# Optimization experiments

Measured on AMD Instinct MI355X. Metric: run time of the kernel, lower is better.

The kernel has to match this reference:

```python
import jax, jax.numpy as jnp
import numpy as np
import math

B, S, D, H = 32, 512, 1024, 1024


def setup_inputs() -> dict:
    key = jax.random.key(0)
    k_feats, k_wih, k_whh, k_bih, k_bhh = jax.random.split(key, 5)
    stdv = 1.0 / math.sqrt(H)
    u = lambda k, shape: jax.random.uniform(k, shape, jnp.float32, -stdv, stdv)
    return {
        "feats": jax.random.normal(k_feats, (B, S, D), jnp.float32),
        "weight_ih": u(k_wih, (3 * H, D)),
        "weight_hh": u(k_whh, (3 * H, H)),
        "bias_ih": u(k_bih, (3 * H,)),
        "bias_hh": u(k_bhh, (3 * H,)),
    }


def reference(feats, weight_ih, weight_hh, bias_ih, bias_hh):
    b, s, d = feats.shape
    h_dim = weight_hh.shape[1]
    # Precompute input projections for all timesteps in one GEMM: [B,S,3H]
    gi_all = jnp.einsum('bsd,gd->bsg', feats, weight_ih) + bias_ih

    def step(h, gi_t):
        gh = h @ weight_hh.T + bias_hh  # [B,3H]
        i_r, i_i, i_n = jnp.split(gi_t, 3, axis=-1)
        h_r, h_i, h_n = jnp.split(gh, 3, axis=-1)
        resetgate = jax.nn.sigmoid(i_r + h_r)
        inputgate = jax.nn.sigmoid(i_i + h_i)
        newgate = jnp.tanh(i_n + resetgate * h_n)
        hy = newgate + inputgate * (h - newgate)
        return hy, hy

    h0 = jnp.zeros((b, h_dim), feats.dtype)
    h_last, outs = jax.lax.scan(step, h0, jnp.swapaxes(gi_all, 0, 1))  # outs: [S,B,H]
    output = jnp.swapaxes(outs, 0, 1)  # [B,S,H]
    return output, h_last
```

## Files before the change

### kernel.cpp

```cpp
#include <hip/hip_runtime.h>

#define B_  32
#define S_  512
#define D_  1024
#define H_  1024
#define G3  3072

typedef __attribute__((ext_vector_type(8))) short  short8;
typedef __attribute__((ext_vector_type(4))) float  floatx4;

__device__ __forceinline__ unsigned short f2bf(float f) {
    unsigned int u = __builtin_bit_cast(unsigned int, f);
    u = (u + 0x7FFFu + ((u >> 16) & 1u)) >> 16;
    return (unsigned short)u;
}
__device__ __forceinline__ float bf2f(unsigned short h) {
    unsigned int u = ((unsigned int)h) << 16;
    return __builtin_bit_cast(float, u);
}
__device__ __forceinline__ float fsigmoid(float x) {
    float e = __builtin_amdgcn_exp2f(-1.4426950408889634f * x);
    return __builtin_amdgcn_rcpf(1.f + e);
}
__device__ __forceinline__ float ftanh(float x) {
    float e = __builtin_amdgcn_exp2f(2.8853900817779268f * x);
    return 1.f - 2.f * __builtin_amdgcn_rcpf(e + 1.f);
}

__global__ __launch_bounds__(256) void convert_kernel(
    const float* __restrict__ wih, const float* __restrict__ whh,
    unsigned short* __restrict__ wih_h,
    unsigned short* __restrict__ whh_h, unsigned short* __restrict__ whh_l,
    unsigned int* __restrict__ hbuf ,
    int* __restrict__ cnt ) {
    int tid = blockIdx.x * 256 + threadIdx.x;
    int i4 = tid * 4;
    if (i4 < 3145728) {
        float4 w = *(const float4*)(wih + i4);
        ushort4 o;
        o.x = f2bf(w.x); o.y = f2bf(w.y); o.z = f2bf(w.z); o.w = f2bf(w.w);
        *(ushort4*)(wih_h + i4) = o;

        float4 v = *(const float4*)(whh + i4);
        ushort4 h;
        h.x = f2bf(v.x); h.y = f2bf(v.y); h.z = f2bf(v.z); h.w = f2bf(v.w);
        ushort4 l;
        l.x = f2bf(v.x - bf2f(h.x)); l.y = f2bf(v.y - bf2f(h.y));
        l.z = f2bf(v.z - bf2f(h.z)); l.w = f2bf(v.w - bf2f(h.w));
        *(ushort4*)(whh_h + i4) = h;
        *(ushort4*)(whh_l + i4) = l;
    }
    if (tid < 16384) {
        uint4 z; z.x = z.y = z.z = z.w = 0;
        *(uint4*)(hbuf + tid * 4) = z;
    }
    if (tid < 32) {
        int4 z4; z4.x = z4.y = z4.z = z4.w = 0;
        *(int4*)(cnt + tid * 4) = z4;
    }
}

#define BM 128
#define BN 128
#define BK 32
#define LDA 40

__global__ __launch_bounds__(256, 2) void gi_gemm(
    const float* __restrict__ feats,
    const unsigned short* __restrict__ wih_h,
    const float* __restrict__ bias_ih,
    unsigned short* __restrict__ gi) {
    __shared__ unsigned short As[BM * LDA];
    __shared__ unsigned short Bs[BN * LDA];

    int bx = blockIdx.x;
    int nb = bx % (G3 / BN);
    int mb = bx / (G3 / BN);
    int m0 = mb * BM, n0 = nb * BN;
    int tid = threadIdx.x;
    int lane = tid & 63, wave = tid >> 6;
    int quad = lane >> 4, l15 = lane & 15;
    int wm = (wave >> 1) * 64, wn = (wave & 1) * 64;

    floatx4 acc[4][4];
#pragma unroll
    for (int i = 0; i < 4; ++i)
#pragma unroll
        for (int j = 0; j < 4; ++j) acc[i][j] = (floatx4){0.f, 0.f, 0.f, 0.f};

    float bias[4];
#pragma unroll
    for (int j = 0; j < 4; ++j) bias[j] = bias_ih[n0 + wn + j * 16 + l15];

    int srow = tid >> 1, shalf = tid & 1;
    const float* aptr = feats + (size_t)(m0 + srow) * D_ + shalf * 16;
    const unsigned short* bptr = wih_h + (size_t)(n0 + srow) * D_ + shalf * 16;
    unsigned short* as = As + srow * LDA + shalf * 16;
    unsigned short* bs = Bs + srow * LDA + shalf * 16;

    for (int kt = 0; kt < D_ / BK; ++kt) {
        int k0 = kt * BK;
        float4 a0 = *(const float4*)(aptr + k0);
        float4 a1 = *(const float4*)(aptr + k0 + 4);
        float4 a2 = *(const float4*)(aptr + k0 + 8);
        float4 a3 = *(const float4*)(aptr + k0 + 12);
        uint4 bA = *(const uint4*)(bptr + k0);
        uint4 bB = *(const uint4*)(bptr + k0 + 8);

        union { unsigned short u16[16]; uint4 v[2]; } pk;
        pk.u16[0] = f2bf(a0.x);  pk.u16[1] = f2bf(a0.y);
        pk.u16[2] = f2bf(a0.z);  pk.u16[3] = f2bf(a0.w);
        pk.u16[4] = f2bf(a1.x);  pk.u16[5] = f2bf(a1.y);
        pk.u16[6] = f2bf(a1.z);  pk.u16[7] = f2bf(a1.w);
        pk.u16[8] = f2bf(a2.x);  pk.u16[9] = f2bf(a2.y);
        pk.u16[10] = f2bf(a2.z); pk.u16[11] = f2bf(a2.w);
        pk.u16[12] = f2bf(a3.x); pk.u16[13] = f2bf(a3.y);
        pk.u16[14] = f2bf(a3.z); pk.u16[15] = f2bf(a3.w);

        *(uint4*)as = pk.v[0];
        *(uint4*)(as + 8) = pk.v[1];
        *(uint4*)bs = bA;
        *(uint4*)(bs + 8) = bB;
        __syncthreads();

        short8 af[4], bf[4];
#pragma unroll
        for (int i = 0; i < 4; ++i)
            af[i] = *(const short8*)(As + (wm + i * 16 + l15) * LDA + quad * 8);
#pragma unroll
        for (int j = 0; j < 4; ++j)
            bf[j] = *(const short8*)(Bs + (wn + j * 16 + l15) * LDA + quad * 8);
#pragma unroll
        for (int i = 0; i < 4; ++i)
#pragma unroll
            for (int j = 0; j < 4; ++j)
                acc[i][j] = __builtin_amdgcn_mfma_f32_16x16x32_bf16(
                    af[i], bf[j], acc[i][j], 0, 0, 0);
        __syncthreads();
    }

#pragma unroll
    for (int i = 0; i < 4; ++i)
#pragma unroll
        for (int j = 0; j < 4; ++j)
#pragma unroll
            for (int r = 0; r < 4; ++r) {
                int m = m0 + wm + i * 16 + quad * 4 + r;
                int n = n0 + wn + j * 16 + l15;
                gi[(size_t)m * G3 + n] = f2bf(acc[i][j][r] + bias[j]);
            }
}

__global__ __launch_bounds__(512, 2) void gru_rec(
    const unsigned short* __restrict__ gi,
    const unsigned short* __restrict__ whh_h,
    const unsigned short* __restrict__ whh_l,
    const float* __restrict__ bias_hh,
    unsigned int* __restrict__ hbuf,
    int* __restrict__ cnt,
    float* __restrict__ out) {
    __shared__ floatx4 parts[8][3][64];

    int jg = blockIdx.x >> 1, mt = blockIdx.x & 1;
    int tid = threadIdx.x;
    int ks = tid >> 6, lane = tid & 63;
    int quad = lane >> 4, l15 = lane & 15;
    int j = jg * 16 + l15;

    short8 wfh[3][4], wfl[3][4];
#pragma unroll
    for (int g = 0; g < 3; ++g)
#pragma unroll
        for (int ki = 0; ki < 4; ++ki) {
            size_t off = (size_t)(g * H_ + j) * H_ + ks * 128 + ki * 32 + quad * 8;
            wfh[g][ki] = *(const short8*)(whh_h + off);
            wfl[g][ki] = *(const short8*)(whh_l + off);
        }

    float bhh[3] = {0.f, 0.f, 0.f};
    float hreg[4] = {0.f, 0.f, 0.f, 0.f};
    if (ks == 0) {
#pragma unroll
        for (int g = 0; g < 3; ++g) bhh[g] = bias_hh[g * H_ + j];
    }

    const int arow = mt * 16 + l15;
    const int kbase = ks * 128 + quad * 8;
    int* const cbase = cnt + mt * 64;

    for (int t = 0; t < S_; ++t) {
        unsigned short giu[3][4];
        if (ks == 0) {
#pragma unroll
            for (int g = 0; g < 3; ++g)
#pragma unroll
                for (int r = 0; r < 4; ++r) {
                    int b = mt * 16 + quad * 4 + r;
                    giu[g][r] = gi[((size_t)b * S_ + t) * G3 + g * H_ + j];
                }
        }

        if (t > 0) {
            if (ks == 0) {
                int v = __hip_atomic_load(cbase + lane, __ATOMIC_RELAXED,
                                          __HIP_MEMORY_SCOPE_AGENT);
                while (!__all(v >= t)) {
                    __builtin_amdgcn_s_sleep(1);
                    v = __hip_atomic_load(cbase + lane, __ATOMIC_RELAXED,
                                          __HIP_MEMORY_SCOPE_AGENT);
                }
            }
            __syncthreads();
        }

        const unsigned int* hc = hbuf + ((t & 1) << 15);
        unsigned int* hn = hbuf + (((t & 1) ^ 1) << 15);

        short8 ah[4], al[4];
#pragma unroll
        for (int ki = 0; ki < 4; ++ki) {
            const unsigned long long* p =
                (const unsigned long long*)(hc + arow * H_ + kbase + ki * 32);
            unsigned long long q[4];
#pragma unroll
            for (int c = 0; c < 4; ++c)
                q[c] = __hip_atomic_load(p + c, __ATOMIC_RELAXED,
                                         __HIP_MEMORY_SCOPE_AGENT);
            short8 av, lv;
#pragma unroll
            for (int c = 0; c < 4; ++c) {
                unsigned int u0 = (unsigned int)q[c];
                unsigned int u1 = (unsigned int)(q[c] >> 32);
                av[2 * c]     = (short)(u0 & 0xffffu);
                av[2 * c + 1] = (short)(u1 & 0xffffu);
                lv[2 * c]     = (short)(u0 >> 16);
                lv[2 * c + 1] = (short)(u1 >> 16);
            }
            ah[ki] = av;
            al[ki] = lv;
        }

        floatx4 acc[3];
#pragma unroll
        for (int g = 0; g < 3; ++g) acc[g] = (floatx4){0.f, 0.f, 0.f, 0.f};
#pragma unroll
        for (int ki = 0; ki < 4; ++ki)
#pragma unroll
            for (int g = 0; g < 3; ++g) {
                acc[g] = __builtin_amdgcn_mfma_f32_16x16x32_bf16(ah[ki], wfh[g][ki], acc[g], 0, 0, 0);
                acc[g] = __builtin_amdgcn_mfma_f32_16x16x32_bf16(ah[ki], wfl[g][ki], acc[g], 0, 0, 0);
                acc[g] = __builtin_amdgcn_mfma_f32_16x16x32_bf16(al[ki], wfh[g][ki], acc[g], 0, 0, 0);
            }
#pragma unroll
        for (int g = 0; g < 3; ++g) parts[ks][g][lane] = acc[g];
        __syncthreads();

        float hy[4];
        if (ks == 0) {
            floatx4 gh[3];
#pragma unroll
            for (int g = 0; g < 3; ++g) {
                floatx4 s = parts[0][g][lane];
#pragma unroll
                for (int w = 1; w < 8; ++w) s += parts[w][g][lane];
                gh[g] = s;
            }
#pragma unroll
            for (int r = 0; r < 4; ++r) {
                int b = mt * 16 + quad * 4 + r;
                float rg = fsigmoid(bf2f(giu[0][r]) + gh[0][r] + bhh[0]);
                float zg = fsigmoid(bf2f(giu[1][r]) + gh[1][r] + bhh[1]);
                float ng = ftanh(bf2f(giu[2][r]) + rg * (gh[2][r] + bhh[2]));
                float h = ng + zg * (hreg[r] - ng);
                hreg[r] = h;
                hy[r] = h;
                unsigned short hh = f2bf(h);
                unsigned int pk = (unsigned int)hh |
                                  ((unsigned int)f2bf(h - bf2f(hh)) << 16);
                __hip_atomic_store(hn + b * H_ + j, pk, __ATOMIC_RELAXED,
                                   __HIP_MEMORY_SCOPE_AGENT);
            }
            asm volatile("s_waitcnt vmcnt(0)" ::: "memory");
            if (tid == 0)
                __hip_atomic_store(cbase + jg, t + 1, __ATOMIC_RELAXED,
                                   __HIP_MEMORY_SCOPE_AGENT);
#pragma unroll
            for (int r = 0; r < 4; ++r) {
                int b = mt * 16 + quad * 4 + r;
                __builtin_nontemporal_store(hy[r], out + ((size_t)b * S_ + t) * H_ + j);
                if (t == S_ - 1)
                    __builtin_nontemporal_store(hy[r], out + (size_t)B_ * S_ * H_ + (size_t)b * H_ + j);
            }
        }
    }
}

extern "C" void kernel_launch(void* const* d_in, const int* in_sizes, int n_in,
                              void* d_out, int out_size, void* d_ws, size_t ws_size,
                              hipStream_t stream) {
    const float* feats = (const float*)d_in[0];
    const float* wih   = (const float*)d_in[1];
    const float* whh   = (const float*)d_in[2];
    const float* bih   = (const float*)d_in[3];
    const float* bhh   = (const float*)d_in[4];
    float* out = (float*)d_out;

    unsigned short* wih_h = (unsigned short*)d_ws;
    unsigned short* whh_h = wih_h + (size_t)3145728;
    unsigned short* whh_l = whh_h + (size_t)3145728;
    unsigned short* gi    = whh_l + (size_t)3145728;
    unsigned int*   hbuf  = (unsigned int*)(gi + (size_t)16384 * G3);
    int*            cnt   = (int*)(hbuf + 65536);

    hipLaunchKernelGGL(convert_kernel, dim3(3072), dim3(256), 0, stream,
                       wih, whh, wih_h, whh_h, whh_l, hbuf, cnt);
    hipLaunchKernelGGL(gi_gemm, dim3(3072), dim3(256), 0, stream,
                       feats, wih_h, bih, gi);

    void* args[] = {(void*)&gi, (void*)&whh_h, (void*)&whh_l,
                    (void*)&bhh, (void*)&hbuf, (void*)&cnt, (void*)&out};
    hipLaunchCooperativeKernel((const void*)gru_rec, dim3(128), dim3(512),
                               args, 0, stream);
}
```

Baseline: 3.457 ms.

## Distribute gate math across four waves and poll per-wave flags directly

The GRU gate epilogue, previously done by wave 0 alone for four batch rows, is now split across four waves that each handle one row. Each wave posts its own completion flag. Every wave spins on just the flags for its K-slice, which replaces the wave-0 poll plus __syncthreads barrier and removes the s_sleep. The partial-sum LDS buffer is double-buffered by timestep so the next step's writes cannot race the current reduction. The aim is a shorter serial critical path per timestep, at the cost of more polling traffic and a larger flag array.

```diff
diff --git a/kernel.cpp b/kernel.cpp
--- a/kernel.cpp
+++ b/kernel.cpp
@@ -54,7 +54,7 @@
         uint4 z; z.x = z.y = z.z = z.w = 0;
         *(uint4*)(hbuf + tid * 4) = z;
     }
-    if (tid < 32) {
+    if (tid < 128) {
         int4 z4; z4.x = z4.y = z4.z = z4.w = 0;
         *(int4*)(cnt + tid * 4) = z4;
     }
@@ -159,7 +159,7 @@
     unsigned int* __restrict__ hbuf,
     int* __restrict__ cnt,
     float* __restrict__ out) {
-    __shared__ floatx4 parts[8][3][64];
+    __shared__ floatx4 parts[2][8][3][64];
 
     int jg = blockIdx.x >> 1, mt = blockIdx.x & 1;
     int tid = threadIdx.x;
@@ -177,40 +177,41 @@
             wfl[g][ki] = *(const short8*)(whh_l + off);
         }
 
-    float bhh[3] = {0.f, 0.f, 0.f};
-    float hreg[4] = {0.f, 0.f, 0.f, 0.f};
-    if (ks == 0) {
-#pragma unroll
-        for (int g = 0; g < 3; ++g) bhh[g] = bias_hh[g * H_ + j];
-    }
-
     const int arow = mt * 16 + l15;
     const int kbase = ks * 128 + quad * 8;
-    int* const cbase = cnt + mt * 64;
+
+    const int q = ks;
+    const bool gater = (ks < 4);
+    const int grow = mt * 16 + quad * 4 + q;
+    float bhh0 = 0.f, bhh1 = 0.f, bhh2 = 0.f, hreg = 0.f;
+    if (gater) {
+        bhh0 = bias_hh[j];
+        bhh1 = bias_hh[H_ + j];
+        bhh2 = bias_hh[2 * H_ + j];
+    }
+
+    int* const pollbase = cnt + mt * 256 + ks * 32;
+    int* const myflag   = cnt + mt * 256 + (jg >> 3) * 32 + (jg & 7) * 4 + q;
 
     for (int t = 0; t < S_; ++t) {
-        unsigned short giu[3][4];
-        if (ks == 0) {
-#pragma unroll
-            for (int g = 0; g < 3; ++g)
-#pragma unroll
-                for (int r = 0; r < 4; ++r) {
-                    int b = mt * 16 + quad * 4 + r;
-                    giu[g][r] = gi[((size_t)b * S_ + t) * G3 + g * H_ + j];
-                }
+        unsigned short giu0 = 0, giu1 = 0, giu2 = 0;
+        if (gater) {
+            size_t gb = ((size_t)grow * S_ + t) * G3 + j;
+            giu0 = gi[gb];
+            giu1 = gi[gb + H_];
+            giu2 = gi[gb + 2 * H_];
         }
 
         if (t > 0) {
-            if (ks == 0) {
-                int v = __hip_atomic_load(cbase + lane, __ATOMIC_RELAXED,
-                                          __HIP_MEMORY_SCOPE_AGENT);
-                while (!__all(v >= t)) {
-                    __builtin_amdgcn_s_sleep(1);
-                    v = __hip_atomic_load(cbase + lane, __ATOMIC_RELAXED,
-                                          __HIP_MEMORY_SCOPE_AGENT);
-                }
-            }
-            __syncthreads();
+            int v = (lane < 32)
+                ? __hip_atomic_load(pollbase + lane, __ATOMIC_RELAXED,
+                                    __HIP_MEMORY_SCOPE_AGENT) : t;
+            while (!__all(v >= t)) {
+                v = (lane < 32)
+                    ? __hip_atomic_load(pollbase + lane, __ATOMIC_RELAXED,
+                                        __HIP_MEMORY_SCOPE_AGENT) : t;
+            }
+            asm volatile("" ::: "memory");
         }
 
         const unsigned int* hc = hbuf + ((t & 1) << 15);
@@ -221,16 +222,16 @@
         for (int ki = 0; ki < 4; ++ki) {
             const unsigned long long* p =
                 (const unsigned long long*)(hc + arow * H_ + kbase + ki * 32);
-            unsigned long long q[4];
+            unsigned long long qd[4];
 #pragma unroll
             for (int c = 0; c < 4; ++c)
-                q[c] = __hip_atomic_load(p + c, __ATOMIC_RELAXED,
-                                         __HIP_MEMORY_SCOPE_AGENT);
+                qd[c] = __hip_atomic_load(p + c, __ATOMIC_RELAXED,
+                                          __HIP_MEMORY_SCOPE_AGENT);
             short8 av, lv;
 #pragma unroll
             for (int c = 0; c < 4; ++c) {
-                unsigned int u0 = (unsigned int)q[c];
-                unsigned int u1 = (unsigned int)(q[c] >> 32);
+                unsigned int u0 = (unsigned int)qd[c];
+                unsigned int u1 = (unsigned int)(qd[c] >> 32);
                 av[2 * c]     = (short)(u0 & 0xffffu);
                 av[2 * c + 1] = (short)(u1 & 0xffffu);
                 lv[2 * c]     = (short)(u0 >> 16);
@@ -251,46 +252,41 @@
                 acc[g] = __builtin_amdgcn_mfma_f32_16x16x32_bf16(ah[ki], wfl[g][ki], acc[g], 0, 0, 0);
                 acc[g] = __builtin_amdgcn_mfma_f32_16x16x32_bf16(al[ki], wfh[g][ki], acc[g], 0, 0, 0);
             }
-#pragma unroll
-        for (int g = 0; g < 3; ++g) parts[ks][g][lane] = acc[g];
+        const int pb = t & 1;
+#pragma unroll
+        for (int g = 0; g < 3; ++g) parts[pb][ks][g][lane] = acc[g];
         __syncthreads();
 
-        float hy[4];
-        if (ks == 0) {
+        if (gater) {
             floatx4 gh[3];
 #pragma unroll
             for (int g = 0; g < 3; ++g) {
-                floatx4 s = parts[0][g][lane];
-#pragma unroll
-                for (int w = 1; w < 8; ++w) s += parts[w][g][lane];
+                floatx4 s = parts[pb][0][g][lane];
+#pragma unroll
+                for (int w = 1; w < 8; ++w) s += parts[pb][w][g][lane];
                 gh[g] = s;
             }
-#pragma unroll
-            for (int r = 0; r < 4; ++r) {
-                int b = mt * 16 + quad * 4 + r;
-                float rg = fsigmoid(bf2f(giu[0][r]) + gh[0][r] + bhh[0]);
-                float zg = fsigmoid(bf2f(giu[1][r]) + gh[1][r] + bhh[1]);
-                float ng = ftanh(bf2f(giu[2][r]) + rg * (gh[2][r] + bhh[2]));
-                float h = ng + zg * (hreg[r] - ng);
-                hreg[r] = h;
-                hy[r] = h;
-                unsigned short hh = f2bf(h);
-                unsigned int pk = (unsigned int)hh |
-                                  ((unsigned int)f2bf(h - bf2f(hh)) << 16);
-                __hip_atomic_store(hn + b * H_ + j, pk, __ATOMIC_RELAXED,
+            float g0 = q < 2 ? (q == 0 ? gh[0][0] : gh[0][1]) : (q == 2 ? gh[0][2] : gh[0][3]);
+            float g1 = q < 2 ? (q == 0 ? gh[1][0] : gh[1][1]) : (q == 2 ? gh[1][2] : gh[1][3]);
+            float g2 = q < 2 ? (q == 0 ? gh[2][0] : gh[2][1]) : (q == 2 ? gh[2][2] : gh[2][3]);
+
+            float rg = fsigmoid(bf2f(giu0) + g0 + bhh0);
+            float zg = fsigmoid(bf2f(giu1) + g1 + bhh1);
+            float ng = ftanh(bf2f(giu2) + rg * (g2 + bhh2));
+            float h = ng + zg * (hreg - ng);
+            hreg = h;
+            unsigned short hh = f2bf(h);
+            unsigned int pk = (unsigned int)hh |
+                              ((unsigned int)f2bf(h - bf2f(hh)) << 16);
+            __hip_atomic_store(hn + grow * H_ + j, pk, __ATOMIC_RELAXED,
+                               __HIP_MEMORY_SCOPE_AGENT);
+            asm volatile("s_waitcnt vmcnt(0)" ::: "memory");
+            if (lane == 0)
+                __hip_atomic_store(myflag, t + 1, __ATOMIC_RELAXED,
                                    __HIP_MEMORY_SCOPE_AGENT);
-            }
-            asm volatile("s_waitcnt vmcnt(0)" ::: "memory");
-            if (tid == 0)
-                __hip_atomic_store(cbase + jg, t + 1, __ATOMIC_RELAXED,
-                                   __HIP_MEMORY_SCOPE_AGENT);
-#pragma unroll
-            for (int r = 0; r < 4; ++r) {
-                int b = mt * 16 + quad * 4 + r;
-                __builtin_nontemporal_store(hy[r], out + ((size_t)b * S_ + t) * H_ + j);
-                if (t == S_ - 1)
-                    __builtin_nontemporal_store(hy[r], out + (size_t)B_ * S_ * H_ + (size_t)b * H_ + j);
-            }
+            out[((size_t)grow * S_ + t) * H_ + j] = h;
+            if (t == S_ - 1)
+                out[(size_t)B_ * S_ * H_ + (size_t)grow * H_ + j] = h;
         }
     }
 }
```

Result: slower. 3.936 ms (+13.9%).
